# Kernel optimization log

Measured on AMD Instinct MI355X. Metric: run time of the kernel, lower is better.

The kernel has to match this reference:

```python
import jax, jax.numpy as jnp
import numpy as np

EPS = 1e-20
TEMP = 0.07
HEAD_DIM = 128


def setup_inputs() -> dict:
    key = jax.random.key(0)
    k1, k2, k3 = jax.random.split(key, 3)
    B, C, T, H, W = 4, 512, 8, 32, 32
    x = jax.random.normal(k1, (B, C, T, H, W), dtype=jnp.float32)
    W_head = jax.random.normal(k2, (C, HEAD_DIM), dtype=jnp.float32) / np.sqrt(C).astype(np.float32)
    b_head = jax.random.normal(k3, (HEAD_DIM,), dtype=jnp.float32) * 0.01
    return {"x": x, "W_head": W_head, "b_head": b_head}


def _forward(x, W_head, b_head):
    B, C, T, H, W = x.shape
    N = H * W
    # linear head over channel dim (equivalent to permute->Linear->permute)
    feats = jnp.einsum('bcthw,cd->bdthw', x, W_head) + b_head[None, :, None, None, None]
    keys = feats.reshape(B, HEAD_DIM, T, N)
    # F.normalize(p=2, dim=1): x / max(||x||, 1e-12)
    norm = jnp.maximum(jnp.linalg.norm(keys, axis=1, keepdims=True), 1e-12)
    keys = keys / norm
    # affinity between consecutive frames: [B, T-1, N, N]
    A = jnp.einsum('bctn,bctm->btnm', keys[:, :, :-1], keys[:, :, 1:])
    A12 = jax.nn.softmax(A / TEMP, axis=-1)                         # forward stochastic mats
    A21 = jax.nn.softmax(jnp.swapaxes(A, -1, -2) / TEMP, axis=-1)   # backward stochastic mats
    A12s = jnp.swapaxes(A12, 0, 1)  # [T-1, B, N, N]
    A21s = jnp.swapaxes(A21, 0, 1)  # [T-1, B, N, N]

    # prefix products P[i] = A12[0] @ A12[1] @ ... @ A12[i]
    def step_p(carry, a):
        c = carry @ a
        return c, c
    _, Ptail = jax.lax.scan(step_p, A12s[0], A12s[1:])
    P = jnp.concatenate([A12s[:1], Ptail], axis=0)  # [T-1, B, N, N]

    # suffix products S[i] = A21[i] @ A21[i-1] @ ... @ A21[0]
    def step_s(carry, a):
        c = a @ carry
        return c, c
    _, Stail = jax.lax.scan(step_s, A21s[0], A21s[1:])
    S = jnp.concatenate([A21s[:1], Stail], axis=0)  # [T-1, B, N, N]

    # cycle walks for i = 1..T-2: aar_i = P[i] @ S[i]
    aars = jnp.matmul(P[1:], S[1:])  # [T-2, B, N, N]
    logits = jnp.log(aars + EPS)
    # cross-entropy with identity targets: loss = logsumexp - logit[n, n]
    lse = jax.nn.logsumexp(logits, axis=-1)                  # [T-2, B, N]
    diag = jnp.diagonal(logits, axis1=-2, axis2=-1)          # [T-2, B, N]
    losses = jnp.mean(lse - diag, axis=(1, 2))               # [T-2]
    preds = jnp.argmax(logits, axis=-1)                      # [T-2, B, N]
    tgt = jnp.arange(N)[None, None, :]
    accs = jnp.mean((preds == tgt).astype(jnp.float32), axis=(1, 2))
    # original returns (loss_of_last_walk, diags); diags exposed as stacked arrays
    return losses[-1], losses, accs


def reference(x, W_head, b_head):
    return _forward(x, W_head, b_head)
```

## Files before the change

### kernel.cpp

```cpp
#include <hip/hip_runtime.h>
#include <cstdint>
#include <cstddef>

typedef unsigned short u16;
typedef unsigned long long u64;
using short8 = __attribute__((ext_vector_type(8))) short;
using f32x4  = __attribute__((ext_vector_type(4))) float;

#define KEXP 20.609929155556620f

__device__ __forceinline__ u16 f2bf(float f) {
  unsigned u = __float_as_uint(f);
  u += 0x7fffu + ((u >> 16) & 1u);
  return (u16)(u >> 16);
}
__device__ __forceinline__ float bf2f(u16 h) { return __uint_as_float(((unsigned)h) << 16); }

typedef const unsigned int GASu32 __attribute__((address_space(1)));
typedef unsigned int LASu32 __attribute__((address_space(3)));

__device__ __forceinline__ void gload16(const u16* src, u16* dstLds) {
  __builtin_amdgcn_global_load_lds((GASu32*)src, (LASu32*)dstLds, 16, 0, 0);
}

struct GemmBatch { const u16* A[24]; const u16* B[24]; u16* C[8]; };
enum { M_HEAD = 0, M_EXP = 1, M_PLAIN = 2, M_AAR = 3 };

__device__ __forceinline__ int lds_off32(int r, int kbyte) {
  int rp = r >> 1;
  int sl = (((r & 1) << 2) | (kbyte >> 4)) ^ (rp & 7);
  return rp * 128 + sl * 16;
}

__global__ __launch_bounds__(256) void transpose_x(const float* __restrict__ x, u16* __restrict__ xT) {
  __shared__ float t[32][33];
  int b = blockIdx.z, c0 = blockIdx.y * 32, s0 = blockIdx.x * 32;
  int tid = threadIdx.x;
  int ci = tid >> 3, s4 = (tid & 7) * 4;
  float4 v = *(const float4*)(x + ((size_t)b * 512 + c0 + ci) * 8192 + s0 + s4);
  t[ci][s4 + 0] = v.x; t[ci][s4 + 1] = v.y; t[ci][s4 + 2] = v.z; t[ci][s4 + 3] = v.w;
  __syncthreads();
  int si = tid >> 3, c4 = (tid & 7) * 4;
  ushort4 o;
  o.x = f2bf(t[c4 + 0][si]); o.y = f2bf(t[c4 + 1][si]);
  o.z = f2bf(t[c4 + 2][si]); o.w = f2bf(t[c4 + 3][si]);
  *(ushort4*)(xT + ((size_t)b * 8192 + s0 + si) * 512 + c0 + c4) = o;
}

__global__ __launch_bounds__(256) void transpose_w(const float* __restrict__ W, u16* __restrict__ Wt) {
  int idx = blockIdx.x * 256 + threadIdx.x;
  int d = idx >> 9, c = idx & 511;
  Wt[idx] = (d < 128) ? f2bf(W[c * 128 + d]) : (u16)0;
}

__global__ __launch_bounds__(256) void normalize_keys(u16* __restrict__ keys) {
  int wv = threadIdx.x >> 6, lane = threadIdx.x & 63;
  int row = blockIdx.x * 4 + wv;
  unsigned* p = (unsigned*)(keys + (size_t)row * 128) + lane;
  unsigned v = *p;
  float a = bf2f((u16)(v & 0xffffu)), b = bf2f((u16)(v >> 16));
  float s = a * a + b * b;
  #pragma unroll
  for (int m = 1; m < 64; m <<= 1) s += __shfl_xor(s, m, 64);
  float sc = 1.f / fmaxf(sqrtf(s), 1e-12f);
  *p = (unsigned)f2bf(a * sc) | ((unsigned)f2bf(b * sc) << 16);
}

__global__ __launch_bounds__(256) void reduce_sums(const float* __restrict__ rsEP, const float* __restrict__ csEP,
                                                   float* __restrict__ rsumE, float* __restrict__ csumE) {
  int idx = blockIdx.x * 256 + threadIdx.x;
  if (idx < 28672) {
    int z = idx >> 10, r = idx & 1023;
    float s = 0.f;
    #pragma unroll
    for (int k = 0; k < 16; ++k) s += rsEP[(size_t)z * 16384 + k * 1024 + r];
    rsumE[z * 1024 + r] = s;
  } else {
    int b2 = idx - 28672;
    int z = b2 >> 10, c = b2 & 1023;
    float s = 0.f;
    #pragma unroll
    for (int k = 0; k < 8; ++k) s += csEP[(size_t)z * 8192 + k * 1024 + c];
    csumE[z * 1024 + c] = s;
  }
}

__global__ __launch_bounds__(256) void k3_t0(const u16* __restrict__ E, const float* __restrict__ rsum,
                                             const float* __restrict__ csum,
                                             u16* __restrict__ P0, u16* __restrict__ S0) {
  int b = blockIdx.z, r = blockIdx.x;
  int zE = b * 7;
  const u16* e = E + ((size_t)zE << 20) + (size_t)r * 1024;
  float rr = 1.f / rsum[zE * 1024 + r];
  int c = threadIdx.x * 4;
  ushort4 v = *(const ushort4*)(e + c);
  float4 cv = *(const float4*)(csum + zE * 1024 + c);
  ushort4 o1, o2;
  float v0 = bf2f(v.x), v1 = bf2f(v.y), v2 = bf2f(v.z), v3 = bf2f(v.w);
  o1.x = f2bf(v0 * rr); o1.y = f2bf(v1 * rr); o1.z = f2bf(v2 * rr); o1.w = f2bf(v3 * rr);
  o2.x = f2bf(v0 / cv.x); o2.y = f2bf(v1 / cv.y); o2.z = f2bf(v2 / cv.z); o2.w = f2bf(v3 / cv.w);
  size_t base = ((size_t)b << 20) + (size_t)r * 1024 + c;
  *(ushort4*)(P0 + base) = o1;
  *(ushort4*)(S0 + base) = o2;
}

__global__ __launch_bounds__(256) void k3_tr(const u16* __restrict__ E, const float* __restrict__ rsum,
                                             const float* __restrict__ csum,
                                             u16* __restrict__ Bp, u16* __restrict__ Bs) {
  __shared__ u16 t[64][66];
  int z = blockIdx.z; int b = z / 6, tt = z % 6 + 1;
  int zE = b * 7 + tt;
  int er0 = blockIdx.x * 64, ec0 = blockIdx.y * 64;
  const u16* e = E + ((size_t)zE << 20);
  int tid = threadIdx.x;
  int ri = tid >> 4, c4 = (tid & 15) * 4;
  #pragma unroll
  for (int p = 0; p < 4; ++p) {
    ushort4 v = *(const ushort4*)(e + (size_t)(er0 + ri + p * 16) * 1024 + ec0 + c4);
    t[ri + p * 16][c4 + 0] = v.x; t[ri + p * 16][c4 + 1] = v.y;
    t[ri + p * 16][c4 + 2] = v.z; t[ri + p * 16][c4 + 3] = v.w;
  }
  __syncthreads();
  size_t outBase = (size_t)(b * 6 + tt - 1) << 20;
  float ir0 = 1.f / rsum[zE * 1024 + er0 + c4 + 0];
  float ir1 = 1.f / rsum[zE * 1024 + er0 + c4 + 1];
  float ir2 = 1.f / rsum[zE * 1024 + er0 + c4 + 2];
  float ir3 = 1.f / rsum[zE * 1024 + er0 + c4 + 3];
  #pragma unroll
  for (int p = 0; p < 4; ++p) {
    int roL = ri + p * 16;
    int ro = ec0 + roL;
    float ic = 1.f / csum[zE * 1024 + ro];
    float v0 = bf2f(t[c4 + 0][roL]), v1 = bf2f(t[c4 + 1][roL]);
    float v2 = bf2f(t[c4 + 2][roL]), v3 = bf2f(t[c4 + 3][roL]);
    ushort4 op, os;
    op.x = f2bf(v0 * ir0); op.y = f2bf(v1 * ir1); op.z = f2bf(v2 * ir2); op.w = f2bf(v3 * ir3);
    os.x = f2bf(v0 * ic);  os.y = f2bf(v1 * ic);  os.z = f2bf(v2 * ic);  os.w = f2bf(v3 * ic);
    size_t off = outBase + (size_t)ro * 1024 + er0 + c4;
    *(ushort4*)(Bp + off) = op;
    *(ushort4*)(Bs + off) = os;
  }
}

#define GB128(T, FA, FB, NA, NB)                                                        \
  {                                                                                     \
    int t_ = (T);                                                                       \
    if (t_ + 1 < nt) {                                                                  \
      if (t_ + 2 < nt) asm volatile("s_waitcnt vmcnt(4)" ::: "memory");                 \
      else             asm volatile("s_waitcnt vmcnt(0)" ::: "memory");                 \
      __builtin_amdgcn_s_barrier();                                                     \
      __builtin_amdgcn_sched_barrier(0);                                                \
      _Pragma("unroll")                                                                 \
      for (int f = 0; f < 4; ++f) {                                                     \
        NA[f] = *(const short8*)((const char*)An + offA[f]);                            \
        NB[f] = *(const short8*)((const char*)Bn + offB[f]);                            \
      }                                                                                 \
      if (t_ + 3 < nt) {                                                                \
        int k0_ = (t_ + 3) << 5;                                                        \
        gload16(srcA0 + k0_, A3 + ldso0);                                               \
        gload16(srcA1 + k0_, A3 + ldso1);                                               \
        gload16(srcB0 + k0_, B3 + ldso0);                                               \
        gload16(srcB1 + k0_, B3 + ldso1);                                               \
      }                                                                                 \
      asm volatile("s_waitcnt lgkmcnt(8)" ::: "memory");                                \
    } else {                                                                            \
      asm volatile("s_waitcnt lgkmcnt(0)" ::: "memory");                                \
    }                                                                                   \
    __builtin_amdgcn_sched_barrier(0);                                                  \
    __builtin_amdgcn_s_setprio(1);                                                      \
    _Pragma("unroll")                                                                   \
    for (int fr = 0; fr < 4; ++fr)                                                      \
      _Pragma("unroll")                                                                 \
      for (int fc2 = 0; fc2 < 4; ++fc2)                                                 \
        acc[fr][fc2] = __builtin_amdgcn_mfma_f32_16x16x32_bf16(FA[fr], FB[fc2],         \
                                                               acc[fr][fc2], 0, 0, 0); \
    __builtin_amdgcn_s_setprio(0);                                                      \
    { u16* tA = Ac; Ac = An; An = A2; A2 = A3; A3 = tA;                                 \
      u16* tB = Bc; Bc = Bn; Bn = B2; B2 = B3; B3 = tB; }                               \
  }

__global__ __launch_bounds__(256) void gemm128(GemmBatch batch) {
  __shared__ u16 AsL[4][4096];
  __shared__ u16 BsL[4][4096];
  int tid = threadIdx.x, lane = tid & 63, wv = tid >> 6;
  int wr = wv >> 1, wc = wv & 1;
  int l15 = lane & 15, kb = (lane >> 4) << 4;

  int swz;
  { int per = (int)gridDim.x >> 3; int id0 = blockIdx.x; swz = (id0 & 7) * per + (id0 >> 3); }
  int z = swz >> 6; int r6 = swz & 63;
  int m0 = (r6 & 7) << 7, n0 = (r6 >> 3) << 7;

  const u16* A = batch.A[z];
  const u16* B = batch.B[z];
  u16* C = batch.C[z];
  const int lda = 1024, ldb = 1024;
  const int nt = 32;

  const u16 *srcA0, *srcA1, *srcB0, *srcB1;
  int ldso0, ldso1;
  {
    int g0 = tid, g1 = 256 + tid;
    int rp0 = g0 >> 3, sp0 = (g0 & 7) ^ (rp0 & 7);
    int r0_ = (rp0 << 1) | (sp0 >> 2), kb0 = (sp0 & 3) * 8;
    int rp1 = g1 >> 3, sp1 = (g1 & 7) ^ (rp1 & 7);
    int r1_ = (rp1 << 1) | (sp1 >> 2), kb1 = (sp1 & 3) * 8;
    srcA0 = A + (size_t)(m0 + r0_) * lda + kb0;
    srcA1 = A + (size_t)(m0 + r1_) * lda + kb1;
    srcB0 = B + (size_t)(n0 + r0_) * ldb + kb0;
    srcB1 = B + (size_t)(n0 + r1_) * ldb + kb1;
    ldso0 = g0 * 8; ldso1 = g1 * 8;
  }
  int offA[4], offB[4];
  #pragma unroll
  for (int f = 0; f < 4; ++f) {
    offA[f] = lds_off32((wr << 6) + (f << 4) + l15, kb);
    offB[f] = lds_off32((wc << 6) + (f << 4) + l15, kb);
  }

  f32x4 acc[4][4] = {};

  u16 *Ac = AsL[0], *An = AsL[1], *A2 = AsL[2], *A3 = AsL[3];
  u16 *Bc = BsL[0], *Bn = BsL[1], *B2 = BsL[2], *B3 = BsL[3];

  gload16(srcA0 +  0, Ac + ldso0); gload16(srcA1 +  0, Ac + ldso1);
  gload16(srcB0 +  0, Bc + ldso0); gload16(srcB1 +  0, Bc + ldso1);
  gload16(srcA0 + 32, An + ldso0); gload16(srcA1 + 32, An + ldso1);
  gload16(srcB0 + 32, Bn + ldso0); gload16(srcB1 + 32, Bn + ldso1);
  gload16(srcA0 + 64, A2 + ldso0); gload16(srcA1 + 64, A2 + ldso1);
  gload16(srcB0 + 64, B2 + ldso0); gload16(srcB1 + 64, B2 + ldso1);
  asm volatile("s_waitcnt vmcnt(8)" ::: "memory");
  __builtin_amdgcn_s_barrier();
  __builtin_amdgcn_sched_barrier(0);
  short8 fa0[4], fb0[4], fa1[4], fb1[4];
  #pragma unroll
  for (int f = 0; f < 4; ++f) {
    fa0[f] = *(const short8*)((const char*)Ac + offA[f]);
    fb0[f] = *(const short8*)((const char*)Bc + offB[f]);
  }

  for (int t = 0; t < nt; t += 2) {
    GB128(t,     fa0, fb0, fa1, fb1);
    GB128(t + 1, fa1, fb1, fa0, fb0);
  }

  #pragma unroll
  for (int fr = 0; fr < 4; ++fr)
    #pragma unroll
    for (int fc = 0; fc < 4; ++fc)
      #pragma unroll
      for (int j = 0; j < 4; ++j) {
        int row = m0 + (wr << 6) + (fr << 4) + ((lane >> 4) << 2) + j;
        int col = n0 + (wc << 6) + (fc << 4) + l15;
        C[(size_t)row * 1024 + col] = f2bf(acc[fr][fc][j]);
      }
}

template <int MODE>
__global__ __launch_bounds__(512, 2) void gemm256(const u16* __restrict__ gA,
                                                  u16* __restrict__ gC, GemmBatch batch,
                                                  const float* __restrict__ bias,
                                                  float* __restrict__ rsP, u64* __restrict__ amP,
                                                  float* __restrict__ diagv,
                                                  float* __restrict__ rsEP, float* __restrict__ csEP) {
  __shared__ u16 AsL[4][8192];
  __shared__ u16 BsL[4][8192];
  int tid = threadIdx.x, lane = tid & 63, wv = tid >> 6;
  int wrM = wv >> 2, wrN = wv & 3;
  int l15 = lane & 15, kb = (lane >> 4) << 4;

  int swz;
  { int per = (int)gridDim.x >> 3; int id0 = blockIdx.x; swz = (id0 & 7) * per + (id0 >> 3); }
  int z, m0, n0;
  if constexpr (MODE == M_HEAD) { z = 0; m0 = swz << 8; n0 = 0; }
  else { z = swz >> 4; int r4 = swz & 15; m0 = (r4 & 3) << 8; n0 = (r4 >> 2) << 8; }

  const u16 *A, *B; u16* C;
  int K, lda, ldb, ldc;
  if constexpr (MODE == M_HEAD) {
    A = gA; B = batch.B[0]; C = gC; K = 512; lda = 512; ldb = 512; ldc = 128;
  } else if constexpr (MODE == M_EXP) {
    int b = z / 7, t = z % 7;
    size_t offA0 = (size_t)(b * 8 + t) * 131072;
    A = gA + offA0; B = gA + offA0 + 131072; C = gC + ((size_t)z << 20);
    K = 128; lda = 128; ldb = 128; ldc = 1024;
  } else {
    A = batch.A[z]; B = batch.B[z]; C = nullptr;
    K = 1024; lda = 1024; ldb = 1024; ldc = 1024;
  }

  const u16 *sA0, *sA1, *sB0, *sB1;
  int d0 = tid * 8, d1 = (512 + tid) * 8;
  {
    int g0 = tid, g1 = 512 + tid;
    int rp0 = g0 >> 3, sp0 = (g0 & 7) ^ (rp0 & 7);
    int r0_ = (rp0 << 1) | (sp0 >> 2), kb0 = (sp0 & 3) * 8;
    int rp1 = g1 >> 3, sp1 = (g1 & 7) ^ (rp1 & 7);
    int r1_ = (rp1 << 1) | (sp1 >> 2), kb1 = (sp1 & 3) * 8;
    sA0 = A + (size_t)(m0 + r0_) * lda + kb0;
    sA1 = A + (size_t)(m0 + r1_) * lda + kb1;
    sB0 = B + (size_t)(n0 + r0_) * ldb + kb0;
    sB1 = B + (size_t)(n0 + r1_) * ldb + kb1;
  }
  int offA[8], offB[4];
  #pragma unroll
  for (int f = 0; f < 8; ++f) offA[f] = lds_off32(wrM * 128 + f * 16 + l15, kb);
  #pragma unroll
  for (int f = 0; f < 4; ++f) offB[f] = lds_off32(wrN * 64 + f * 16 + l15, kb);

  f32x4 acc[8][4] = {};
  int nt = K >> 5;

  gload16(sA0,      AsL[0] + d0); gload16(sA1,      AsL[0] + d1);
  gload16(sB0,      BsL[0] + d0); gload16(sB1,      BsL[0] + d1);
  gload16(sA0 + 32, AsL[1] + d0); gload16(sA1 + 32, AsL[1] + d1);
  gload16(sB0 + 32, BsL[1] + d0); gload16(sB1 + 32, BsL[1] + d1);
  asm volatile("s_waitcnt vmcnt(4)" ::: "memory");
  __builtin_amdgcn_s_barrier();

  for (int t = 0; t < nt; ++t) {
    const u16* At = AsL[t & 3];
    const u16* Bt = BsL[t & 3];
    u16* Ad = AsL[(t + 2) & 3];
    u16* Bd = BsL[(t + 2) & 3];
    int k2 = (t + 2) << 5;
    bool st = (t + 2) < nt;
    short8 aF[4], bF[4];
    #pragma unroll
    for (int f = 0; f < 4; ++f) bF[f] = *(const short8*)((const char*)Bt + offB[f]);
    #pragma unroll
    for (int f = 0; f < 4; ++f) aF[f] = *(const short8*)((const char*)At + offA[f]);
    if (st) { gload16(sA0 + k2, Ad + d0); gload16(sA1 + k2, Ad + d1); }
    __builtin_amdgcn_sched_barrier(0);
    __builtin_amdgcn_s_barrier();
    asm volatile("s_waitcnt lgkmcnt(0)" ::: "memory");
    __builtin_amdgcn_sched_barrier(0);
    __builtin_amdgcn_s_setprio(1);
    #pragma unroll
    for (int fa = 0; fa < 4; ++fa)
      #pragma unroll
      for (int fb = 0; fb < 4; ++fb)
        acc[fa][fb] = __builtin_amdgcn_mfma_f32_16x16x32_bf16(aF[fa], bF[fb], acc[fa][fb], 0, 0, 0);
    __builtin_amdgcn_s_setprio(0);
    __builtin_amdgcn_sched_barrier(0);
    __builtin_amdgcn_s_barrier();
    #pragma unroll
    for (int f = 0; f < 4; ++f) aF[f] = *(const short8*)((const char*)At + offA[4 + f]);
    if (st) { gload16(sB0 + k2, Bd + d0); gload16(sB1 + k2, Bd + d1); }
    if (st) asm volatile("s_waitcnt vmcnt(4)" ::: "memory");
    else    asm volatile("s_waitcnt vmcnt(0)" ::: "memory");
    __builtin_amdgcn_sched_barrier(0);
    __builtin_amdgcn_s_barrier();
    asm volatile("s_waitcnt lgkmcnt(0)" ::: "memory");
    __builtin_amdgcn_sched_barrier(0);
    __builtin_amdgcn_s_setprio(1);
    #pragma unroll
    for (int fa = 0; fa < 4; ++fa)
      #pragma unroll
      for (int fb = 0; fb < 4; ++fb)
        acc[4 + fa][fb] = __builtin_amdgcn_mfma_f32_16x16x32_bf16(aF[fa], bF[fb], acc[4 + fa][fb], 0, 0, 0);
    __builtin_amdgcn_s_setprio(0);
    __builtin_amdgcn_sched_barrier(0);
    __builtin_amdgcn_s_barrier();
  }

  if constexpr (MODE == M_AAR) {
    int nb = n0 >> 8;
    size_t pbase = (size_t)z * 16384 + (size_t)((nb << 2) | wrN) * 1024;
    #pragma unroll
    for (int fa = 0; fa < 8; ++fa) {
      #pragma unroll
      for (int j = 0; j < 4; ++j) {
        float rs = 0.f, mv = -1.f; int mc = 0;
        #pragma unroll
        for (int fb = 0; fb < 4; ++fb) {
          float v = acc[fa][fb][j];
          rs += v;
          int c = n0 + (wrN << 6) + (fb << 4) + l15;
          if (v > mv) { mv = v; mc = c; }
        }
        u64 pk = ((u64)__float_as_uint(mv) << 32) | (u64)(unsigned)(1023 - mc);
        #pragma unroll
        for (int m = 1; m < 16; m <<= 1) {
          rs += __shfl_xor(rs, m, 64);
          u64 o = __shfl_xor(pk, m, 64);
          pk = (o > pk) ? o : pk;
        }
        if (l15 == 0) {
          int row = m0 + (wrM << 7) + (fa << 4) + ((lane >> 4) << 2) + j;
          rsP[pbase + row] = rs;
          amP[pbase + row] = pk;
        }
      }
      if (m0 == n0 && wrN == ((wrM << 1) | (fa >> 2))) {
        int fb = fa & 3;
        int jj = l15 - ((lane >> 4) << 2);
        if (jj >= 0 && jj < 4) {
          int row = m0 + (wrM << 7) + (fa << 4) + l15;
          float dv = (jj == 0) ? acc[fa][fb][0] : (jj == 1) ? acc[fa][fb][1]
                    : (jj == 2) ? acc[fa][fb][2] : acc[fa][fb][3];
          diagv[(z << 10) + row] = dv;
        }
      }
    }
  } else if constexpr (MODE == M_EXP) {
    float rp_[8][4] = {};
    float cp_[4] = {};
    #pragma unroll
    for (int fa = 0; fa < 8; ++fa)
      #pragma unroll
      for (int fb = 0; fb < 4; ++fb)
        #pragma unroll
        for (int j = 0; j < 4; ++j) {
          int row = m0 + (wrM << 7) + (fa << 4) + ((lane >> 4) << 2) + j;
          int col = n0 + (wrN << 6) + (fb << 4) + l15;
          float v = exp2f(acc[fa][fb][j] * KEXP);
          C[(size_t)row * ldc + col] = f2bf(v);
          rp_[fa][j] += v;
          cp_[fb] += v;
        }
    int nb = n0 >> 8, mb = m0 >> 8;
    size_t rbase = (size_t)z * 16384 + (size_t)((nb << 2) | wrN) * 1024;
    size_t cbase = (size_t)z * 8192 + (size_t)((mb << 1) | wrM) * 1024;
    #pragma unroll
    for (int fa = 0; fa < 8; ++fa)
      #pragma unroll
      for (int j = 0; j < 4; ++j) {
        float r = rp_[fa][j];
        r += __shfl_xor(r, 1, 64); r += __shfl_xor(r, 2, 64);
        r += __shfl_xor(r, 4, 64); r += __shfl_xor(r, 8, 64);
        if (l15 == 0) {
          int row = m0 + (wrM << 7) + (fa << 4) + ((lane >> 4) << 2) + j;
          rsEP[rbase + row] = r;
        }
      }
    #pragma unroll
    for (int fb = 0; fb < 4; ++fb) {
      float c = cp_[fb];
      c += __shfl_xor(c, 16, 64); c += __shfl_xor(c, 32, 64);
      if ((lane >> 4) == 0) {
        int col = n0 + (wrN << 6) + (fb << 4) + l15;
        csEP[cbase + col] = c;
      }
    }
  } else {
    if (wrN < 2) {
      float bv[4];
      #pragma unroll
      for (int fb = 0; fb < 4; ++fb) bv[fb] = bias[(wrN << 6) + (fb << 4) + l15];
      #pragma unroll
      for (int fa = 0; fa < 8; ++fa)
        #pragma unroll
        for (int fb = 0; fb < 4; ++fb)
          #pragma unroll
          for (int j = 0; j < 4; ++j) {
            int row = m0 + (wrM << 7) + (fa << 4) + ((lane >> 4) << 2) + j;
            int col = (wrN << 6) + (fb << 4) + l15;
            C[(size_t)row * 128 + col] = f2bf(acc[fa][fb][j] + bv[fb]);
          }
    }
  }
}

__global__ __launch_bounds__(256) void finalize_k(const float* __restrict__ rsP, const u64* __restrict__ amP,
                                                  const float* __restrict__ diagv, float* __restrict__ out) {
  __shared__ float sl[256], sa[256];
  int w = blockIdx.x;
  int tid = threadIdx.x;
  float ls = 0.f, ac = 0.f;
  for (int idx = tid; idx < 4096; idx += 256) {
    int b = idx >> 10, n = idx & 1023;
    int z = (w << 2) + b;
    size_t base = (size_t)z * 16384 + n;
    float rs = 0.f; u64 pk = 0;
    #pragma unroll
    for (int k = 0; k < 16; ++k) {
      rs += rsP[base + k * 1024];
      u64 o = amP[base + k * 1024];
      pk = (o > pk) ? o : pk;
    }
    float dv = diagv[(z << 10) + n];
    ls += logf(rs + 1024.f * 1e-20f) - logf(dv + 1e-20f);
    unsigned pred = 1023u - (unsigned)(pk & 0xffffffffULL);
    ac += (pred == (unsigned)n) ? 1.f : 0.f;
  }
  sl[tid] = ls; sa[tid] = ac;
  __syncthreads();
  for (int s2 = 128; s2 > 0; s2 >>= 1) {
    if (tid < s2) { sl[tid] += sl[tid + s2]; sa[tid] += sa[tid + s2]; }
    __syncthreads();
  }
  if (tid == 0) {
    float loss = sl[0] / 4096.f, acv = sa[0] / 4096.f;
    out[1 + w] = loss;
    out[7 + w] = acv;
    if (w == 5) out[0] = loss;
  }
}

extern "C" void kernel_launch(void* const* d_in, const int* in_sizes, int n_in,
                              void* d_out, int out_size, void* d_ws, size_t ws_size,
                              hipStream_t stream) {
  (void)in_sizes; (void)n_in; (void)out_size; (void)ws_size;
  const float* x  = (const float*)d_in[0];
  const float* Wh = (const float*)d_in[1];
  const float* bh = (const float*)d_in[2];
  float* out = (float*)d_out;
  char* ws = (char*)d_ws;
  const size_t MB = 1ull << 20;

  u16* xT   = (u16*)(ws);
  u16* keys = (u16*)(ws + 32 * MB);
  float* rsP   = (float*)(ws + 32 * MB);
  u64*   amP   = (u64*)(ws + 34 * MB);
  float* diagv = (float*)(ws + 38 * MB);
  u16* WtP  = (u16*)(ws + 40 * MB);
  float* rsumE = (float*)(ws + 40 * MB + 288 * 1024);
  float* csumE = (float*)(ws + 40 * MB + 416 * 1024);
  u16* E    = (u16*)(ws + 41 * MB);
  float* rsEP  = (float*)(ws + 113 * MB);
  float* csEP  = (float*)(ws + 116 * MB);
  u16* Bp   = (u16*)(ws + 113 * MB);
  u16* Bs   = (u16*)(ws + 161 * MB);

  u16* Pb[7] = { (u16*)(ws + 97 * MB), (u16*)(ws + 0 * MB), (u16*)(ws + 8 * MB),
                 (u16*)(ws + 16 * MB), (u16*)(ws + 24 * MB), (u16*)(ws + 41 * MB),
                 (u16*)(ws + 49 * MB) };
  u16* Sb[7] = { (u16*)(ws + 105 * MB), (u16*)(ws + 57 * MB), (u16*)(ws + 65 * MB),
                 (u16*)(ws + 73 * MB), (u16*)(ws + 81 * MB), (u16*)(ws + 89 * MB),
                 (u16*)(ws + 97 * MB) };

  GemmBatch empty{};

  transpose_x<<<dim3(256, 16, 4), 256, 0, stream>>>(x, xT);
  transpose_w<<<dim3(512), 256, 0, stream>>>(Wh, WtP);
  {
    GemmBatch hb{}; hb.B[0] = WtP;
    gemm256<M_HEAD><<<dim3(128), 512, 0, stream>>>(xT, keys, hb, bh,
                                                   nullptr, nullptr, nullptr, nullptr, nullptr);
  }
  normalize_keys<<<dim3(8192), 256, 0, stream>>>(keys);
  gemm256<M_EXP><<<dim3(448), 512, 0, stream>>>(keys, E, empty, nullptr,
                                                nullptr, nullptr, nullptr, rsEP, csEP);
  reduce_sums<<<dim3(224), 256, 0, stream>>>(rsEP, csEP, rsumE, csumE);
  k3_t0<<<dim3(1024, 1, 4), 256, 0, stream>>>(E, rsumE, csumE, Pb[0], Sb[0]);
  k3_tr<<<dim3(16, 16, 24), 256, 0, stream>>>(E, rsumE, csumE, Bp, Bs);

  for (int i = 1; i <= 6; ++i) {
    GemmBatch gb{};
    for (int b = 0; b < 4; ++b) {
      gb.A[b]     = Pb[i - 1] + (size_t)b * 1048576;
      gb.B[b]     = Bp + (size_t)(b * 6 + i - 1) * 1048576;
      gb.C[b]     = Pb[i] + (size_t)b * 1048576;
      gb.A[4 + b] = Sb[i - 1] + (size_t)b * 1048576;
      gb.B[4 + b] = Bs + (size_t)(b * 6 + i - 1) * 1048576;
      gb.C[4 + b] = Sb[i] + (size_t)b * 1048576;
    }
    gemm128<<<dim3(512), 256, 0, stream>>>(gb);
  }

  GemmBatch ga{};
  for (int i = 1; i <= 6; ++i)
    for (int b = 0; b < 4; ++b) {
      ga.A[(i - 1) * 4 + b] = Pb[i] + (size_t)b * 1048576;
      ga.B[(i - 1) * 4 + b] = Sb[i] + (size_t)b * 1048576;
    }
  gemm256<M_AAR><<<dim3(384), 512, 0, stream>>>(nullptr, nullptr, ga, nullptr,
                                                rsP, amP, diagv, nullptr, nullptr);
  finalize_k<<<dim3(6), 256, 0, stream>>>(rsP, amP, diagv, out);
}
```

Before: 337.5 us.

## Replace 4-stage split-phase GEMM pipeline with simple double buffering

Replaces the hand-scheduled main loop of the 256x256 GEMM kernel with a plain double-buffered loop. The old loop used a 4-deep LDS ring, interleaved half-tile MFMA phases, sched_barriers and setprio. The new loop issues the next tile's global-to-LDS loads, reads all fragments, runs all MFMAs and then does one __syncthreads per K step. It also halves LDS use and drops the min-2-blocks launch bound, which may allow more registers per thread or more blocks per CU. In exchange it risks exposing load latency, and correctness depends on the async LDS loads having completed by the time __syncthreads is reached.

Result: slower. 362.6 us (+7.4%).

```diff
diff --git a/kernel.cpp b/kernel.cpp
--- a/kernel.cpp
+++ b/kernel.cpp
@@ -257,14 +257,14 @@
 }
 
 template <int MODE>
-__global__ __launch_bounds__(512, 2) void gemm256(const u16* __restrict__ gA,
-                                                  u16* __restrict__ gC, GemmBatch batch,
-                                                  const float* __restrict__ bias,
-                                                  float* __restrict__ rsP, u64* __restrict__ amP,
-                                                  float* __restrict__ diagv,
-                                                  float* __restrict__ rsEP, float* __restrict__ csEP) {
-  __shared__ u16 AsL[4][8192];
-  __shared__ u16 BsL[4][8192];
+__global__ __launch_bounds__(512) void gemm256(const u16* __restrict__ gA,
+                                               u16* __restrict__ gC, GemmBatch batch,
+                                               const float* __restrict__ bias,
+                                               float* __restrict__ rsP, u64* __restrict__ amP,
+                                               float* __restrict__ diagv,
+                                               float* __restrict__ rsEP, float* __restrict__ csEP) {
+  __shared__ u16 AsL[2][8192];
+  __shared__ u16 BsL[2][8192];
   int tid = threadIdx.x, lane = tid & 63, wv = tid >> 6;
   int wrM = wv >> 2, wrN = wv & 3;
   int l15 = lane & 15, kb = (lane >> 4) << 4;
@@ -311,57 +311,31 @@
   f32x4 acc[8][4] = {};
   int nt = K >> 5;
 
-  gload16(sA0,      AsL[0] + d0); gload16(sA1,      AsL[0] + d1);
-  gload16(sB0,      BsL[0] + d0); gload16(sB1,      BsL[0] + d1);
-  gload16(sA0 + 32, AsL[1] + d0); gload16(sA1 + 32, AsL[1] + d1);
-  gload16(sB0 + 32, BsL[1] + d0); gload16(sB1 + 32, BsL[1] + d1);
-  asm volatile("s_waitcnt vmcnt(4)" ::: "memory");
-  __builtin_amdgcn_s_barrier();
-
+  gload16(sA0, AsL[0] + d0); gload16(sA1, AsL[0] + d1);
+  gload16(sB0, BsL[0] + d0); gload16(sB1, BsL[0] + d1);
+  __syncthreads();
+
+  int cur = 0;
   for (int t = 0; t < nt; ++t) {
-    const u16* At = AsL[t & 3];
-    const u16* Bt = BsL[t & 3];
-    u16* Ad = AsL[(t + 2) & 3];
-    u16* Bd = BsL[(t + 2) & 3];
-    int k2 = (t + 2) << 5;
-    bool st = (t + 2) < nt;
-    short8 aF[4], bF[4];
+    const u16* At = AsL[cur];
+    const u16* Bt = BsL[cur];
+    if (t + 1 < nt) {
+      int k1 = (t + 1) << 5;
+      gload16(sA0 + k1, AsL[cur ^ 1] + d0); gload16(sA1 + k1, AsL[cur ^ 1] + d1);
+      gload16(sB0 + k1, BsL[cur ^ 1] + d0); gload16(sB1 + k1, BsL[cur ^ 1] + d1);
+    }
+    short8 aF[8], bF[4];
+    #pragma unroll
+    for (int f = 0; f < 8; ++f) aF[f] = *(const short8*)((const char*)At + offA[f]);
     #pragma unroll
     for (int f = 0; f < 4; ++f) bF[f] = *(const short8*)((const char*)Bt + offB[f]);
     #pragma unroll
-    for (int f = 0; f < 4; ++f) aF[f] = *(const short8*)((const char*)At + offA[f]);
-    if (st) { gload16(sA0 + k2, Ad + d0); gload16(sA1 + k2, Ad + d1); }
-    __builtin_amdgcn_sched_barrier(0);
-    __builtin_amdgcn_s_barrier();
-    asm volatile("s_waitcnt lgkmcnt(0)" ::: "memory");
-    __builtin_amdgcn_sched_barrier(0);
-    __builtin_amdgcn_s_setprio(1);
-    #pragma unroll
-    for (int fa = 0; fa < 4; ++fa)
+    for (int fa = 0; fa < 8; ++fa)
       #pragma unroll
       for (int fb = 0; fb < 4; ++fb)
         acc[fa][fb] = __builtin_amdgcn_mfma_f32_16x16x32_bf16(aF[fa], bF[fb], acc[fa][fb], 0, 0, 0);
-    __builtin_amdgcn_s_setprio(0);
-    __builtin_amdgcn_sched_barrier(0);
-    __builtin_amdgcn_s_barrier();
-    #pragma unroll
-    for (int f = 0; f < 4; ++f) aF[f] = *(const short8*)((const char*)At + offA[4 + f]);
-    if (st) { gload16(sB0 + k2, Bd + d0); gload16(sB1 + k2, Bd + d1); }
-    if (st) asm volatile("s_waitcnt vmcnt(4)" ::: "memory");
-    else    asm volatile("s_waitcnt vmcnt(0)" ::: "memory");
-    __builtin_amdgcn_sched_barrier(0);
-    __builtin_amdgcn_s_barrier();
-    asm volatile("s_waitcnt lgkmcnt(0)" ::: "memory");
-    __builtin_amdgcn_sched_barrier(0);
-    __builtin_amdgcn_s_setprio(1);
-    #pragma unroll
-    for (int fa = 0; fa < 4; ++fa)
-      #pragma unroll
-      for (int fb = 0; fb < 4; ++fb)
-        acc[4 + fa][fb] = __builtin_amdgcn_mfma_f32_16x16x32_bf16(aF[fa], bF[fb], acc[4 + fa][fb], 0, 0, 0);
-    __builtin_amdgcn_s_setprio(0);
-    __builtin_amdgcn_sched_barrier(0);
-    __builtin_amdgcn_s_barrier();
+    __syncthreads();
+    cur ^= 1;
   }
 
   if constexpr (MODE == M_AAR) {
```
